# Kernel optimization log

Hardware: AMD Instinct MI355X
Metric: run time of the kernel (lower is better)

The kernel has to match this reference:

```python
import jax, jax.numpy as jnp
import numpy as np

N_NODES = 50000
N_EDGES = 800000
D_IN = 128
D_OUT = 128


def setup_inputs() -> dict:
    key = jax.random.key(0)
    k1, k2, k3, k4, k5, k6 = jax.random.split(key, 6)
    curr_fea = jax.random.normal(k1, (N_NODES, D_IN), dtype=jnp.float32)
    edge_index = jax.random.randint(k2, (2, N_EDGES), 0, N_NODES, dtype=jnp.int64)
    s = 1.0 / np.sqrt(D_IN)
    W_self = jax.random.uniform(k3, (D_OUT, D_IN), jnp.float32, -s, s)
    b_self = jax.random.uniform(k4, (D_OUT,), jnp.float32, -s, s)
    W_neig = jax.random.uniform(k5, (D_OUT, D_IN), jnp.float32, -s, s)
    b_neig = jax.random.uniform(k6, (D_OUT,), jnp.float32, -s, s)
    return {"curr_fea": curr_fea, "edge_index": edge_index,
            "W_self": W_self, "b_self": b_self,
            "W_neig": W_neig, "b_neig": b_neig}


def reference(curr_fea, edge_index, W_self, b_self, W_neig, b_neig):
    num_nodes = curr_fea.shape[0]
    src, dst = edge_index[0], edge_index[1]
    # symmetrize: messages flow both directions
    src_all = jnp.concatenate([src, dst], axis=0)  # [2E]
    dst_all = jnp.concatenate([dst, src], axis=0)  # [2E]
    # gather neighbor features then scatter-add into destination nodes
    nei_sum = jax.ops.segment_sum(curr_fea[src_all], dst_all,
                                  num_segments=num_nodes)  # [N, d]
    out = (curr_fea @ W_self.T + b_self) + (nei_sum @ W_neig.T + b_neig)
    return out
```

## Files before the change

kernel.cpp:

```cpp
#include <hip/hip_runtime.h>

#define DD 128
#define BM 64
#define BK 32
#define BKN 64
#define NPB 32
#define NBMAX 1024
#define ECH 2048
#define CAP 2304
#define PADC 136

typedef __attribute__((ext_vector_type(8))) short bf16x8;
typedef __attribute__((ext_vector_type(4))) float f32x4;

__device__ __forceinline__ unsigned short f2b(float x) {
    unsigned u = __float_as_uint(x);
    u += 0x7fffu + ((u >> 16) & 1u);
    return (unsigned short)(u >> 16);
}
__device__ __forceinline__ float b2f_lo(unsigned v) { return __uint_as_float(v << 16); }
__device__ __forceinline__ float b2f_hi(unsigned v) { return __uint_as_float(v & 0xffff0000u); }
__device__ __forceinline__ float bf(unsigned short u) {
    return __uint_as_float((unsigned)u << 16);
}

__device__ __forceinline__ int detect_rf(const void* ei_raw, int E, int lane) {
    const unsigned long long* p = (const unsigned long long*)ei_raw;
    int n64 = E < 64 ? E : 64;
    bool big = (lane < n64) && (p[lane] >= (1ULL << 32));
    return (__ballot(big) == 0ULL) ? 1 : 0;
}

__global__ void detect_kernel(const unsigned long long* __restrict__ ei,
                              int n64, int* __restrict__ flag) {
    int i = threadIdx.x;
    bool big = (i < n64) && (ei[i] >= (1ULL << 32));
    unsigned long long b = __ballot(big);
    if (i == 0) *flag = (b == 0ULL) ? 1 : 0;
}

__global__ void cvt_all_kernel(const float* __restrict__ fea,
                               const float* __restrict__ Ws,
                               const float* __restrict__ Wn,
                               unsigned short* __restrict__ feaB,
                               unsigned short* __restrict__ Wcat, int n4) {
    int i = blockIdx.x * 256 + threadIdx.x;
    if (i < n4) {
        float4 v = reinterpret_cast<const float4*>(fea)[i];
        ushort4 o;
        o.x = f2b(v.x); o.y = f2b(v.y); o.z = f2b(v.z); o.w = f2b(v.w);
        reinterpret_cast<ushort4*>(feaB)[i] = o;
    } else if (i < n4 + 2 * DD * DD / 4) {
        int k4 = i - n4;
        int n = k4 >> 6;
        int kk = (k4 & 63) * 4;
        float4 v = (kk < DD) ? *reinterpret_cast<const float4*>(Ws + n * DD + kk)
                             : *reinterpret_cast<const float4*>(Wn + n * DD + kk - DD);
        ushort4 o;
        o.x = f2b(v.x); o.y = f2b(v.y); o.z = f2b(v.z); o.w = f2b(v.w);
        reinterpret_cast<ushort4*>(Wcat)[k4] = o;
    }
}

__global__ void cvt_fea_kernel(const float* __restrict__ in,
                               unsigned short* __restrict__ out, int n4) {
    int i = blockIdx.x * 256 + threadIdx.x;
    if (i >= n4) return;
    float4 v = reinterpret_cast<const float4*>(in)[i];
    ushort4 o;
    o.x = f2b(v.x); o.y = f2b(v.y); o.z = f2b(v.z); o.w = f2b(v.w);
    reinterpret_cast<ushort4*>(out)[i] = o;
}

__global__ void cvt_w_kernel(const float* __restrict__ Ws,
                             const float* __restrict__ Wn,
                             unsigned short* __restrict__ Wcat) {
    int i = blockIdx.x * 256 + threadIdx.x;
    int n = i >> 8, k = i & 255;
    float v = (k < DD) ? Ws[n * DD + k] : Wn[n * DD + (k - DD)];
    Wcat[i] = f2b(v);
}

__launch_bounds__(512)
__global__ void bin_kernel(const void* __restrict__ ei_raw, int E,
                           unsigned* __restrict__ region,
                           unsigned* __restrict__ gcur, int nbk) {
    __shared__ unsigned stage[2 * ECH];
    __shared__ unsigned cnt[NBMAX];
    __shared__ unsigned start[NBMAX];
    __shared__ unsigned cursor[NBMAX];
    __shared__ unsigned gbase[NBMAX];
    __shared__ unsigned scanT[512];

    const int t = threadIdx.x;
    const int lane = t & 63;
    const int rf = detect_rf(ei_raw, E, lane);

    for (int b = t; b < NBMAX; b += 512) { cnt[b] = 0; cursor[b] = 0; }
    __syncthreads();

    const int e0 = blockIdx.x * ECH;
    int es[4], ed[4];
#pragma unroll
    for (int j = 0; j < 4; ++j) {
        int e = e0 + j * 512 + t;
        if (e < E) {
            if (rf) {
                const long long* p = (const long long*)ei_raw;
                es[j] = (int)p[e]; ed[j] = (int)p[e + E];
            } else {
                const int* p = (const int*)ei_raw;
                es[j] = p[e]; ed[j] = p[e + E];
            }
            atomicAdd(&cnt[ed[j] >> 6], 1u);
            atomicAdd(&cnt[es[j] >> 6], 1u);
        } else {
            es[j] = -1; ed[j] = -1;
        }
    }
    __syncthreads();

    unsigned lv[2]; unsigned lsum = 0;
#pragma unroll
    for (int j = 0; j < 2; ++j) { lv[j] = cnt[t * 2 + j]; lsum += lv[j]; }
    scanT[t] = lsum; __syncthreads();
    for (int o = 1; o < 512; o <<= 1) {
        unsigned x = (t >= o) ? scanT[t - o] : 0;
        __syncthreads();
        scanT[t] += x;
        __syncthreads();
    }
    unsigned run = scanT[t] - lsum;
#pragma unroll
    for (int j = 0; j < 2; ++j) { start[t * 2 + j] = run; run += lv[j]; }
    __syncthreads();

#pragma unroll
    for (int j = 0; j < 4; ++j) {
        if (es[j] >= 0) {
            int s = es[j], d = ed[j];
            unsigned p0 = atomicAdd(&cursor[d >> 6], 1u);
            stage[start[d >> 6] + p0] = (unsigned)(d & 63) | ((unsigned)s << 6);
            unsigned p1 = atomicAdd(&cursor[s >> 6], 1u);
            stage[start[s >> 6] + p1] = (unsigned)(s & 63) | ((unsigned)d << 6);
        }
    }
    __syncthreads();

    for (int b = t; b < nbk; b += 512) {
        unsigned c = cnt[b];
        gbase[b] = c ? atomicAdd(&gcur[b], c) : 0;
    }
    __syncthreads();

    const int w = t >> 6;
    for (int b = w; b < nbk; b += 8) {
        unsigned c = cnt[b];
        if (!c) continue;
        unsigned gb = gbase[b], st = start[b];
        for (unsigned l2 = lane; l2 < c; l2 += 64) {
            unsigned idx = gb + l2;
            if (idx < CAP)
                region[(size_t)b * CAP + idx] = stage[st + l2];
        }
    }
}

__launch_bounds__(256)
__global__ void gather_gemm2_kernel(const unsigned short* __restrict__ feaB,
                                    const unsigned short* __restrict__ Wcat,
                                    const unsigned* __restrict__ region,
                                    const unsigned* __restrict__ gcur,
                                    const float* __restrict__ bs,
                                    const float* __restrict__ bn,
                                    float* __restrict__ out, int M) {
    __shared__ unsigned srt[CAP];
    __shared__ unsigned short neiL[NPB][PADC];
    __shared__ unsigned c64[BKN];
    __shared__ unsigned p64[BKN];
    __shared__ unsigned cur64[BKN];

    const int t = threadIdx.x;
    const int b2 = blockIdx.x, b = b2 >> 1, h = b2 & 1;
    unsigned cnt = gcur[b];
    if (cnt > CAP) cnt = CAP;
    const unsigned* reg = region + (size_t)b * CAP;

    unsigned ent[9];
#pragma unroll
    for (int q = 0; q < 9; ++q) {
        unsigned i = (unsigned)t + (unsigned)q * 256u;
        ent[q] = (i < cnt) ? reg[i] : 0xFFFFFFFFu;
    }

    if (t < BKN) { c64[t] = 0; cur64[t] = 0; }
    __syncthreads();

#pragma unroll
    for (int q = 0; q < 9; ++q)
        if (ent[q] != 0xFFFFFFFFu) atomicAdd(&c64[ent[q] & 63u], 1u);
    __syncthreads();

    if (t < 64) {
        unsigned v = c64[t];
        unsigned sc = v;
#pragma unroll
        for (int o = 1; o < 64; o <<= 1) {
            unsigned x = __shfl_up(sc, o, 64);
            if (t >= o) sc += x;
        }
        p64[t] = sc - v;
    }
    __syncthreads();

#pragma unroll
    for (int q = 0; q < 9; ++q) {
        if (ent[q] != 0xFFFFFFFFu) {
            unsigned e = ent[q];
            unsigned p = atomicAdd(&cur64[e & 63u], 1u);
            srt[p64[e & 63u] + p] = e >> 6;
        }
    }
    __syncthreads();

    const int w = t >> 6, lane = t & 63;
    const int half = lane >> 5, li = lane & 31;
    const unsigned short* bp = feaB + li * 4;

    for (int n = h * NPB + w; n < h * NPB + NPB; n += 4) {
        int g = b * BKN + n;
        unsigned p = p64[n];
        unsigned d = (g < M) ? c64[n] : 0;
        float a0 = 0.f, a1 = 0.f, a2 = 0.f, a3 = 0.f;
        unsigned j = 0;
        for (; j + 16 <= d; j += 16) {
            ushort4 v[8];
#pragma unroll
            for (int q = 0; q < 8; ++q) {
                unsigned s = srt[p + j + 2 * q + half];
                v[q] = *reinterpret_cast<const ushort4*>(bp + (size_t)s * DD);
            }
#pragma unroll
            for (int q = 0; q < 8; ++q) {
                a0 += bf(v[q].x); a1 += bf(v[q].y);
                a2 += bf(v[q].z); a3 += bf(v[q].w);
            }
        }
        for (; j + 2 <= d; j += 2) {
            unsigned s = srt[p + j + half];
            ushort4 v = *reinterpret_cast<const ushort4*>(bp + (size_t)s * DD);
            a0 += bf(v.x); a1 += bf(v.y); a2 += bf(v.z); a3 += bf(v.w);
        }
        if (j < d && half == 0) {
            unsigned s = srt[p + j];
            ushort4 v = *reinterpret_cast<const ushort4*>(bp + (size_t)s * DD);
            a0 += bf(v.x); a1 += bf(v.y); a2 += bf(v.z); a3 += bf(v.w);
        }
        a0 += __shfl_xor(a0, 32);
        a1 += __shfl_xor(a1, 32);
        a2 += __shfl_xor(a2, 32);
        a3 += __shfl_xor(a3, 32);
        if (half == 0) {
            ushort4 o;
            o.x = f2b(a0); o.y = f2b(a1); o.z = f2b(a2); o.w = f2b(a3);
            *reinterpret_cast<ushort4*>(&neiL[n - h * NPB][li * 4]) = o;
        }
    }
    __syncthreads();

    const int lr = lane & 15, ks = lane >> 4;
    const int rg = w & 1, cgr = w >> 1;
    const int row0 = b2 * NPB + rg * 16;
    const int rowl = rg * 16 + lr;
    const int rowg = row0 + lr;
    const int col0 = cgr * 64;

    f32x4 acc[4] = {};
#pragma unroll
    for (int kb = 0; kb < 256; kb += 32) {
        bf16x8 a;
        if (kb < DD) {
            if (rowg < M)
                a = *reinterpret_cast<const bf16x8*>(
                    feaB + (size_t)rowg * DD + kb + ks * 8);
            else
                a = bf16x8{0, 0, 0, 0, 0, 0, 0, 0};
        } else {
            a = *reinterpret_cast<const bf16x8*>(&neiL[rowl][(kb - DD) + ks * 8]);
        }
#pragma unroll
        for (int ci = 0; ci < 4; ++ci) {
            int nn = col0 + ci * 16 + lr;
            bf16x8 bb = *reinterpret_cast<const bf16x8*>(
                Wcat + (size_t)nn * 256 + kb + ks * 8);
            acc[ci] = __builtin_amdgcn_mfma_f32_16x16x32_bf16(a, bb, acc[ci], 0, 0, 0);
        }
    }

#pragma unroll
    for (int ci = 0; ci < 4; ++ci) {
        int colg = col0 + ci * 16 + lr;
        float bias = bs[colg] + bn[colg];
        int rbase = row0 + ks * 4;
#pragma unroll
        for (int i2 = 0; i2 < 4; ++i2) {
            int r2 = rbase + i2;
            if (r2 < M) out[(size_t)r2 * DD + colg] = acc[ci][i2] + bias;
        }
    }
}

__global__ void transpose_kernel(const float* __restrict__ Ws,
                                 const float* __restrict__ Wn,
                                 float* __restrict__ Wts,
                                 float* __restrict__ Wtn) {
    int idx = blockIdx.x * blockDim.x + threadIdx.x;
    int i = idx & (DD * DD - 1);
    int col = i >> 7;
    int k = i & (DD - 1);
    if (idx < DD * DD)          Wts[k * DD + col] = Ws[i];
    else if (idx < 2 * DD * DD) Wtn[k * DD + col] = Wn[i];
}

__global__ void hist_kernel(const void* __restrict__ ei_raw,
                            int* __restrict__ deg, int E,
                            const int* __restrict__ flag) {
    int e = blockIdx.x * 256 + threadIdx.x;
    if (e >= E) return;
    int s, d;
    if (*flag) {
        const long long* ei = (const long long*)ei_raw;
        s = (int)ei[e]; d = (int)ei[e + E];
    } else {
        const int* ei = (const int*)ei_raw;
        s = ei[e]; d = ei[e + E];
    }
    atomicAdd(&deg[s], 1);
    atomicAdd(&deg[d], 1);
}

__global__ void scan1_kernel(const int* __restrict__ deg, int* __restrict__ off,
                             int* __restrict__ bsum, int N) {
    __shared__ int sd[256];
    int base = blockIdx.x * 1024;
    int t = threadIdx.x;
    int v[4]; int s = 0;
#pragma unroll
    for (int j = 0; j < 4; ++j) {
        int idx = base + t * 4 + j;
        v[j] = (idx < N) ? deg[idx] : 0;
        s += v[j];
    }
    sd[t] = s; __syncthreads();
    for (int o = 1; o < 256; o <<= 1) {
        int x = (t >= o) ? sd[t - o] : 0;
        __syncthreads();
        sd[t] += x;
        __syncthreads();
    }
    int run = sd[t] - s;
    if (t == 255) bsum[blockIdx.x] = sd[255];
#pragma unroll
    for (int j = 0; j < 4; ++j) {
        int idx = base + t * 4 + j;
        if (idx < N) off[idx] = run;
        run += v[j];
    }
}

__global__ void scan2_kernel(int* __restrict__ bsum, int NB,
                             int* __restrict__ total) {
    __shared__ int sd[256];
    int t = threadIdx.x;
    int v = (t < NB) ? bsum[t] : 0;
    sd[t] = v; __syncthreads();
    for (int o = 1; o < 256; o <<= 1) {
        int x = (t >= o) ? sd[t - o] : 0;
        __syncthreads();
        sd[t] += x;
        __syncthreads();
    }
    if (t < NB) bsum[t] = sd[t] - v;
    if (t == 255) *total = sd[255];
}

__global__ void scan3_kernel(int* __restrict__ off, const int* __restrict__ bsum,
                             int N) {
    int i = blockIdx.x * blockDim.x + threadIdx.x;
    if (i < N) off[i] += bsum[i >> 10];
}

__global__ void fill_kernel(const void* __restrict__ ei_raw,
                            const int* __restrict__ off,
                            int* __restrict__ cursor, int* __restrict__ list,
                            int E, const int* __restrict__ flag) {
    int e = blockIdx.x * 256 + threadIdx.x;
    if (e >= E) return;
    int s, d;
    if (*flag) {
        const long long* ei = (const long long*)ei_raw;
        s = (int)ei[e]; d = (int)ei[e + E];
    } else {
        const int* ei = (const int*)ei_raw;
        s = ei[e]; d = ei[e + E];
    }
    int p0 = atomicAdd(&cursor[d], 1); list[off[d] + p0] = s;
    int p1 = atomicAdd(&cursor[s], 1); list[off[s] + p1] = d;
}

__launch_bounds__(256)
__global__ void gather_b_kernel(const unsigned short* __restrict__ feaB,
                                const int* __restrict__ off,
                                const int* __restrict__ list,
                                unsigned short* __restrict__ neiB, int N) {
    int w = (int)((blockIdx.x * 256 + threadIdx.x) >> 6);
    if (w >= N) return;
    int lane = threadIdx.x & 63;
    int start = off[w], end = off[w + 1];
    float ax = 0.f, ay = 0.f;
    const unsigned short* base = feaB + lane * 2;
    int j = start;
    for (; j + 4 <= end; j += 4) {
        int s0 = list[j], s1 = list[j + 1], s2 = list[j + 2], s3 = list[j + 3];
        unsigned a = *reinterpret_cast<const unsigned*>(base + (size_t)s0 * DD);
        unsigned b = *reinterpret_cast<const unsigned*>(base + (size_t)s1 * DD);
        unsigned c = *reinterpret_cast<const unsigned*>(base + (size_t)s2 * DD);
        unsigned d = *reinterpret_cast<const unsigned*>(base + (size_t)s3 * DD);
        ax += b2f_lo(a) + b2f_lo(b) + b2f_lo(c) + b2f_lo(d);
        ay += b2f_hi(a) + b2f_hi(b) + b2f_hi(c) + b2f_hi(d);
    }
    for (; j < end; ++j) {
        unsigned a = *reinterpret_cast<const unsigned*>(base + (size_t)list[j] * DD);
        ax += b2f_lo(a); ay += b2f_hi(a);
    }
    ushort2 o; o.x = f2b(ax); o.y = f2b(ay);
    *reinterpret_cast<ushort2*>(neiB + (size_t)w * DD + lane * 2) = o;
}

__launch_bounds__(256)
__global__ void gather_f32_kernel(const float* __restrict__ fea,
                                  const int* __restrict__ off,
                                  const int* __restrict__ list,
                                  float* __restrict__ nei, int N) {
    int w = (int)((blockIdx.x * 256 + threadIdx.x) >> 6);
    if (w >= N) return;
    int lane = threadIdx.x & 63;
    int start = off[w], end = off[w + 1];
    float2 acc = make_float2(0.f, 0.f);
    const float* base = fea + (size_t)lane * 2;
    int j = start;
    for (; j + 4 <= end; j += 4) {
        int s0 = list[j], s1 = list[j + 1], s2 = list[j + 2], s3 = list[j + 3];
        float2 a = *reinterpret_cast<const float2*>(base + (size_t)s0 * DD);
        float2 b = *reinterpret_cast<const float2*>(base + (size_t)s1 * DD);
        float2 c = *reinterpret_cast<const float2*>(base + (size_t)s2 * DD);
        float2 e = *reinterpret_cast<const float2*>(base + (size_t)s3 * DD);
        acc.x += a.x + b.x + c.x + e.x;
        acc.y += a.y + b.y + c.y + e.y;
    }
    for (; j < end; ++j) {
        float2 a = *reinterpret_cast<const float2*>(base + (size_t)list[j] * DD);
        acc.x += a.x; acc.y += a.y;
    }
    *reinterpret_cast<float2*>(nei + (size_t)w * DD + lane * 2) = acc;
}

__global__ void scatter_kernel(const float* __restrict__ fea,
                               const void* __restrict__ ei_raw,
                               float* __restrict__ nei,
                               int E, const int* __restrict__ flag) {
    long long r = (long long)blockIdx.x * 8 + (threadIdx.x >> 5);
    if (r >= 2LL * E) return;
    int lr = threadIdx.x & 31;
    int i = (int)(r < E ? r : r - E);
    int s, d;
    if (*flag) {
        const long long* ei = (const long long*)ei_raw;
        s = (int)ei[i]; d = (int)ei[i + E];
    } else {
        const int* ei = (const int*)ei_raw;
        s = ei[i]; d = ei[i + E];
    }
    if (r >= E) { int t = s; s = d; d = t; }
    const float4 v = *reinterpret_cast<const float4*>(fea + (size_t)s * DD + lr * 4);
    float* p = nei + (size_t)d * DD + lr * 4;
    unsafeAtomicAdd(p + 0, v.x);
    unsafeAtomicAdd(p + 1, v.y);
    unsafeAtomicAdd(p + 2, v.z);
    unsafeAtomicAdd(p + 3, v.w);
}

__launch_bounds__(256)
__global__ void gemm_mfma_kernel(const unsigned short* __restrict__ feaB,
                                 const unsigned short* __restrict__ neiB,
                                 const unsigned short* __restrict__ Wcat,
                                 const float* __restrict__ bs,
                                 const float* __restrict__ bn,
                                 float* __restrict__ out, int M) {
    const int w  = threadIdx.x >> 6;
    const int l  = threadIdx.x & 63;
    const int lr = l & 15;
    const int ks = l >> 4;
    const int row0 = blockIdx.x * 128 + w * 32;
    const int col0 = blockIdx.y * 64;

    f32x4 acc[2][4] = {};

#pragma unroll
    for (int kb = 0; kb < 256; kb += 32) {
        const unsigned short* A = (kb < DD) ? feaB : neiB;
        const int klocal = (kb < DD) ? kb : kb - DD;
        bf16x8 a[2];
#pragma unroll
        for (int ri = 0; ri < 2; ++ri) {
            int rowg = row0 + ri * 16 + lr;
            if (rowg < M)
                a[ri] = *reinterpret_cast<const bf16x8*>(
                    A + (size_t)rowg * DD + klocal + ks * 8);
            else
                a[ri] = bf16x8{0, 0, 0, 0, 0, 0, 0, 0};
        }
#pragma unroll
        for (int ci = 0; ci < 4; ++ci) {
            int n = col0 + ci * 16 + lr;
            bf16x8 b = *reinterpret_cast<const bf16x8*>(
                Wcat + (size_t)n * 256 + kb + ks * 8);
#pragma unroll
            for (int ri = 0; ri < 2; ++ri)
                acc[ri][ci] = __builtin_amdgcn_mfma_f32_16x16x32_bf16(
                    a[ri], b, acc[ri][ci], 0, 0, 0);
        }
    }

#pragma unroll
    for (int ci = 0; ci < 4; ++ci) {
        int colg = col0 + ci * 16 + lr;
        float bias = bs[colg] + bn[colg];
#pragma unroll
        for (int ri = 0; ri < 2; ++ri) {
            int rbase = row0 + ri * 16 + ks * 4;
#pragma unroll
            for (int i = 0; i < 4; ++i) {
                int rowg = rbase + i;
                if (rowg < M)
                    out[(size_t)rowg * DD + colg] = acc[ri][ci][i] + bias;
            }
        }
    }
}

__launch_bounds__(256)
__global__ void gemm_kernel(const float* __restrict__ fea,
                            const float* __restrict__ nei,
                            const float* __restrict__ Wts,
                            const float* __restrict__ Wtn,
                            const float* __restrict__ bs,
                            const float* __restrict__ bn,
                            float* __restrict__ out, int M) {
    __shared__ float Fs[BM][BK + 4];
    __shared__ float Ns[BM][BK + 4];
    __shared__ float WsT[BK][DD];
    __shared__ float WnT[BK][DD];

    const int t = threadIdx.x;
    const int cg = t & 31;
    const int rg = t >> 5;
    const int row0 = blockIdx.x * BM;

    float4 acc[8];
#pragma unroll
    for (int r = 0; r < 8; ++r) acc[r] = make_float4(0.f, 0.f, 0.f, 0.f);

    for (int kb = 0; kb < DD; kb += BK) {
#pragma unroll
        for (int j = 0; j < 2; ++j) {
            int idx = t + j * 256;
            int row = idx >> 3;
            int seg = idx & 7;
            int grow = row0 + row;
            float4 fv = make_float4(0.f, 0.f, 0.f, 0.f);
            float4 nv = make_float4(0.f, 0.f, 0.f, 0.f);
            if (grow < M) {
                fv = *reinterpret_cast<const float4*>(fea + (size_t)grow * DD + kb + seg * 4);
                nv = *reinterpret_cast<const float4*>(nei + (size_t)grow * DD + kb + seg * 4);
            }
            *reinterpret_cast<float4*>(&Fs[row][seg * 4]) = fv;
            *reinterpret_cast<float4*>(&Ns[row][seg * 4]) = nv;
        }
#pragma unroll
        for (int j = 0; j < 4; ++j) {
            int idx = t + j * 256;
            int kk = idx >> 5;
            int seg = idx & 31;
            *reinterpret_cast<float4*>(&WsT[kk][seg * 4]) =
                *reinterpret_cast<const float4*>(Wts + (size_t)(kb + kk) * DD + seg * 4);
            *reinterpret_cast<float4*>(&WnT[kk][seg * 4]) =
                *reinterpret_cast<const float4*>(Wtn + (size_t)(kb + kk) * DD + seg * 4);
        }
        __syncthreads();

#pragma unroll
        for (int kk = 0; kk < BK; ++kk) {
            float4 wsv = *reinterpret_cast<const float4*>(&WsT[kk][cg * 4]);
            float4 wnv = *reinterpret_cast<const float4*>(&WnT[kk][cg * 4]);
#pragma unroll
            for (int r = 0; r < 8; ++r) {
                float a = Fs[rg * 8 + r][kk];
                float b = Ns[rg * 8 + r][kk];
                acc[r].x += a * wsv.x + b * wnv.x;
                acc[r].y += a * wsv.y + b * wnv.y;
                acc[r].z += a * wsv.z + b * wnv.z;
                acc[r].w += a * wsv.w + b * wnv.w;
            }
        }
        __syncthreads();
    }

    float4 bsv = *reinterpret_cast<const float4*>(bs + cg * 4);
    float4 bnv = *reinterpret_cast<const float4*>(bn + cg * 4);
    float4 bias = make_float4(bsv.x + bnv.x, bsv.y + bnv.y, bsv.z + bnv.z, bsv.w + bnv.w);
#pragma unroll
    for (int r = 0; r < 8; ++r) {
        int grow = row0 + rg * 8 + r;
        if (grow < M) {
            float4 o = make_float4(acc[r].x + bias.x, acc[r].y + bias.y,
                                   acc[r].z + bias.z, acc[r].w + bias.w);
            *reinterpret_cast<float4*>(out + (size_t)grow * DD + cg * 4) = o;
        }
    }
}

extern "C" void kernel_launch(void* const* d_in, const int* in_sizes, int n_in,
                              void* d_out, int out_size, void* d_ws, size_t ws_size,
                              hipStream_t stream) {
    const float* fea = (const float*)d_in[0];
    const void*  ei  = d_in[1];
    const float* Ws  = (const float*)d_in[2];
    const float* bsv = (const float*)d_in[3];
    const float* Wn  = (const float*)d_in[4];
    const float* bnv = (const float*)d_in[5];

    const int M = in_sizes[0] / DD;
    const int E = in_sizes[1] / 2;
    float* out = (float*)d_out;
    char* ws = (char*)d_ws;
    int* flag = (int*)ws;

    const int NBK = (M + BKN - 1) / BKN;
    const size_t csr_bytes = (size_t)M * 8 + (size_t)(M + 1) * 4 + 4096
                           + (size_t)2 * E * 4;

    size_t o1 = 256;
    unsigned short* Wcat = (unsigned short*)(ws + o1); o1 += (size_t)DD * 256 * 2;
    unsigned short* feaB = (unsigned short*)(ws + o1); o1 += (size_t)M * DD * 2;
    unsigned* gcur  = (unsigned*)(ws + o1);            o1 += 4096;
    unsigned* region = (unsigned*)(ws + o1);           o1 += (size_t)NBK * CAP * 4;
    size_t need1 = o1;

    size_t o2 = 256 + (size_t)DD * 256 * 2 + (size_t)M * DD * 2;
    unsigned short* neiB2 = (unsigned short*)(ws + o2);
    size_t o2b = o2 + (size_t)M * DD * 2;
    size_t need2 = o2b + csr_bytes;

    size_t o3 = 256;
    float* Wts = (float*)(ws + o3); o3 += (size_t)DD * DD * 4;
    float* Wtn = (float*)(ws + o3); o3 += (size_t)DD * DD * 4;
    size_t need3 = o3 + csr_bytes;

    const int NB = (M + 1023) / 1024;
    const int eb = (E + 255) / 256;
    const int n4 = M * DD / 4;

    if (ws_size >= need1 && NBK <= NBMAX) {
        hipMemsetAsync(gcur, 0, 4096, stream);
        int cvtb = (n4 + 2 * DD * DD / 4 + 255) / 256;
        cvt_all_kernel<<<cvtb, 256, 0, stream>>>(fea, Ws, Wn, feaB, Wcat, n4);
        int abks = (E + ECH - 1) / ECH;
        bin_kernel<<<abks, 512, 0, stream>>>(ei, E, region, gcur, NBK);
        gather_gemm2_kernel<<<2 * NBK, 256, 0, stream>>>(feaB, Wcat, region, gcur,
                                                         bsv, bnv, out, M);
    } else if (ws_size >= need2) {
        int* deg    = (int*)(ws + o2b);
        int* cursor = deg + M;
        int* off    = cursor + M;
        int* bsum   = off + (M + 1);
        int* list   = bsum + 1024;

        detect_kernel<<<1, 64, 0, stream>>>((const unsigned long long*)ei,
                                            E < 64 ? E : 64, flag);
        cvt_fea_kernel<<<(n4 + 255) / 256, 256, 0, stream>>>(fea, feaB, n4);
        cvt_w_kernel<<<(DD * 256 + 255) / 256, 256, 0, stream>>>(Ws, Wn, Wcat);
        hipMemsetAsync(deg, 0, (size_t)2 * M * 4, stream);
        hist_kernel<<<eb, 256, 0, stream>>>(ei, deg, E, flag);
        scan1_kernel<<<NB, 256, 0, stream>>>(deg, off, bsum, M);
        scan2_kernel<<<1, 256, 0, stream>>>(bsum, NB, &off[M]);
        scan3_kernel<<<(M + 255) / 256, 256, 0, stream>>>(off, bsum, M);
        fill_kernel<<<eb, 256, 0, stream>>>(ei, off, cursor, list, E, flag);
        gather_b_kernel<<<(M + 3) / 4, 256, 0, stream>>>(feaB, off, list, neiB2, M);
        dim3 g((M + 127) / 128, 2);
        gemm_mfma_kernel<<<g, 256, 0, stream>>>(feaB, neiB2, Wcat, bsv, bnv, out, M);
    } else if (ws_size >= need3) {
        int* deg    = (int*)(ws + o3);
        int* cursor = deg + M;
        int* off    = cursor + M;
        int* bsum   = off + (M + 1);
        int* list   = bsum + 1024;
        float* nei = out;

        detect_kernel<<<1, 64, 0, stream>>>((const unsigned long long*)ei,
                                            E < 64 ? E : 64, flag);
        transpose_kernel<<<(2 * DD * DD + 255) / 256, 256, 0, stream>>>(Ws, Wn, Wts, Wtn);
        hipMemsetAsync(deg, 0, (size_t)2 * M * 4, stream);
        hist_kernel<<<eb, 256, 0, stream>>>(ei, deg, E, flag);
        scan1_kernel<<<NB, 256, 0, stream>>>(deg, off, bsum, M);
        scan2_kernel<<<1, 256, 0, stream>>>(bsum, NB, &off[M]);
        scan3_kernel<<<(M + 255) / 256, 256, 0, stream>>>(off, bsum, M);
        fill_kernel<<<eb, 256, 0, stream>>>(ei, off, cursor, list, E, flag);
        gather_f32_kernel<<<(M + 3) / 4, 256, 0, stream>>>(fea, off, list, nei, M);
        gemm_kernel<<<(M + BM - 1) / BM, 256, 0, stream>>>(fea, nei, Wts, Wtn,
                                                           bsv, bnv, out, M);
    } else {
        float* nei = out;
        detect_kernel<<<1, 64, 0, stream>>>((const unsigned long long*)ei,
                                            E < 64 ? E : 64, flag);
        transpose_kernel<<<(2 * DD * DD + 255) / 256, 256, 0, stream>>>(Ws, Wn, Wts, Wtn);
        hipMemsetAsync(nei, 0, (size_t)M * DD * 4, stream);
        long long rows = 2LL * E;
        int sblocks = (int)((rows + 7) / 8);
        scatter_kernel<<<sblocks, 256, 0, stream>>>(fea, ei, nei, E, flag);
        gemm_kernel<<<(M + BM - 1) / BM, 256, 0, stream>>>(fea, nei, Wts, Wtn,
                                                           bsv, bnv, out, M);
    }
}
```

Measured before the change: 199.6 us.

## Fuse bf16 conversion into binning kernel and widen neighbor gather loads

```diff
diff --git a/kernel.cpp b/kernel.cpp
--- a/kernel.cpp
+++ b/kernel.cpp
@@ -12,6 +12,7 @@
 
 typedef __attribute__((ext_vector_type(8))) short bf16x8;
 typedef __attribute__((ext_vector_type(4))) float f32x4;
+typedef __attribute__((ext_vector_type(8))) unsigned short u16x8;
 
 __device__ __forceinline__ unsigned short f2b(float x) {
     unsigned u = __float_as_uint(x);
@@ -37,29 +38,6 @@
     bool big = (i < n64) && (ei[i] >= (1ULL << 32));
     unsigned long long b = __ballot(big);
     if (i == 0) *flag = (b == 0ULL) ? 1 : 0;
-}
-
-__global__ void cvt_all_kernel(const float* __restrict__ fea,
-                               const float* __restrict__ Ws,
-                               const float* __restrict__ Wn,
-                               unsigned short* __restrict__ feaB,
-                               unsigned short* __restrict__ Wcat, int n4) {
-    int i = blockIdx.x * 256 + threadIdx.x;
-    if (i < n4) {
-        float4 v = reinterpret_cast<const float4*>(fea)[i];
-        ushort4 o;
-        o.x = f2b(v.x); o.y = f2b(v.y); o.z = f2b(v.z); o.w = f2b(v.w);
-        reinterpret_cast<ushort4*>(feaB)[i] = o;
-    } else if (i < n4 + 2 * DD * DD / 4) {
-        int k4 = i - n4;
-        int n = k4 >> 6;
-        int kk = (k4 & 63) * 4;
-        float4 v = (kk < DD) ? *reinterpret_cast<const float4*>(Ws + n * DD + kk)
-                             : *reinterpret_cast<const float4*>(Wn + n * DD + kk - DD);
-        ushort4 o;
-        o.x = f2b(v.x); o.y = f2b(v.y); o.z = f2b(v.z); o.w = f2b(v.w);
-        reinterpret_cast<ushort4*>(Wcat)[k4] = o;
-    }
 }
 
 __global__ void cvt_fea_kernel(const float* __restrict__ in,
@@ -82,9 +60,14 @@
 }
 
 __launch_bounds__(512)
-__global__ void bin_kernel(const void* __restrict__ ei_raw, int E,
-                           unsigned* __restrict__ region,
-                           unsigned* __restrict__ gcur, int nbk) {
+__global__ void binc_kernel(const void* __restrict__ ei_raw, int E,
+                            unsigned* __restrict__ region,
+                            unsigned* __restrict__ gcur, int nbk, int abks,
+                            const float* __restrict__ fea,
+                            const float* __restrict__ Ws,
+                            const float* __restrict__ Wn,
+                            unsigned short* __restrict__ feaB,
+                            unsigned short* __restrict__ Wcat, int n4) {
     __shared__ unsigned stage[2 * ECH];
     __shared__ unsigned cnt[NBMAX];
     __shared__ unsigned start[NBMAX];
@@ -93,6 +76,27 @@
     __shared__ unsigned scanT[512];
 
     const int t = threadIdx.x;
+
+    if (blockIdx.x >= abks) {
+        int i = (blockIdx.x - abks) * 512 + t;
+        if (i < n4) {
+            float4 v = reinterpret_cast<const float4*>(fea)[i];
+            ushort4 o;
+            o.x = f2b(v.x); o.y = f2b(v.y); o.z = f2b(v.z); o.w = f2b(v.w);
+            reinterpret_cast<ushort4*>(feaB)[i] = o;
+        } else if (i < n4 + 2 * DD * DD / 4) {
+            int k4 = i - n4;
+            int n = k4 >> 6;
+            int kk = (k4 & 63) * 4;
+            float4 v = (kk < DD) ? *reinterpret_cast<const float4*>(Ws + n * DD + kk)
+                                 : *reinterpret_cast<const float4*>(Wn + n * DD + kk - DD);
+            ushort4 o;
+            o.x = f2b(v.x); o.y = f2b(v.y); o.z = f2b(v.z); o.w = f2b(v.w);
+            reinterpret_cast<ushort4*>(Wcat)[k4] = o;
+        }
+        return;
+    }
+
     const int lane = t & 63;
     const int rf = detect_rf(ei_raw, E, lane);
 
@@ -224,49 +228,65 @@
     __syncthreads();
 
     const int w = t >> 6, lane = t & 63;
-    const int half = lane >> 5, li = lane & 31;
-    const unsigned short* bp = feaB + li * 4;
+    const int grp = lane >> 4, li16 = lane & 15;
+    const unsigned short* bp = feaB + li16 * 8;
 
     for (int n = h * NPB + w; n < h * NPB + NPB; n += 4) {
         int g = b * BKN + n;
         unsigned p = p64[n];
         unsigned d = (g < M) ? c64[n] : 0;
-        float a0 = 0.f, a1 = 0.f, a2 = 0.f, a3 = 0.f;
+        float a[8] = {0.f, 0.f, 0.f, 0.f, 0.f, 0.f, 0.f, 0.f};
         unsigned j = 0;
+        for (; j + 32 <= d; j += 32) {
+            u16x8 v[8];
+#pragma unroll
+            for (int q = 0; q < 8; ++q) {
+                unsigned s = srt[p + j + 4 * q + grp];
+                v[q] = *reinterpret_cast<const u16x8*>(bp + (size_t)s * DD);
+            }
+#pragma unroll
+            for (int q = 0; q < 8; ++q) {
+#pragma unroll
+                for (int c = 0; c < 8; ++c) a[c] += bf(v[q][c]);
+            }
+        }
         for (; j + 16 <= d; j += 16) {
-            ushort4 v[8];
-#pragma unroll
-            for (int q = 0; q < 8; ++q) {
-                unsigned s = srt[p + j + 2 * q + half];
-                v[q] = *reinterpret_cast<const ushort4*>(bp + (size_t)s * DD);
+            u16x8 v[4];
+#pragma unroll
+            for (int q = 0; q < 4; ++q) {
+                unsigned s = srt[p + j + 4 * q + grp];
+                v[q] = *reinterpret_cast<const u16x8*>(bp + (size_t)s * DD);
             }
 #pragma unroll
-            for (int q = 0; q < 8; ++q) {
-                a0 += bf(v[q].x); a1 += bf(v[q].y);
-                a2 += bf(v[q].z); a3 += bf(v[q].w);
+            for (int q = 0; q < 4; ++q) {
+#pragma unroll
+                for (int c = 0; c < 8; ++c) a[c] += bf(v[q][c]);
             }
         }
-        for (; j + 2 <= d; j += 2) {
-            unsigned s = srt[p + j + half];
-            ushort4 v = *reinterpret_cast<const ushort4*>(bp + (size_t)s * DD);
-            a0 += bf(v.x); a1 += bf(v.y); a2 += bf(v.z); a3 += bf(v.w);
-        }
-        if (j < d && half == 0) {
-            unsigned s = srt[p + j];
-            ushort4 v = *reinterpret_cast<const ushort4*>(bp + (size_t)s * DD);
-            a0 += bf(v.x); a1 += bf(v.y); a2 += bf(v.z); a3 += bf(v.w);
-        }
-        a0 += __shfl_xor(a0, 32);
-        a1 += __shfl_xor(a1, 32);
-        a2 += __shfl_xor(a2, 32);
-        a3 += __shfl_xor(a3, 32);
-        if (half == 0) {
-            ushort4 o;
-            o.x = f2b(a0); o.y = f2b(a1); o.z = f2b(a2); o.w = f2b(a3);
-            *reinterpret_cast<ushort4*>(&neiL[n - h * NPB][li * 4]) = o;
-        }
-    }
-    __syncthreads();
+        for (; j + 4 <= d; j += 4) {
+            unsigned s = srt[p + j + grp];
+            u16x8 v = *reinterpret_cast<const u16x8*>(bp + (size_t)s * DD);
+#pragma unroll
+            for (int c = 0; c < 8; ++c) a[c] += bf(v[c]);
+        }
+        if (j < d && grp < (int)(d - j)) {
+            unsigned s = srt[p + j + grp];
+            u16x8 v = *reinterpret_cast<const u16x8*>(bp + (size_t)s * DD);
+#pragma unroll
+            for (int c = 0; c < 8; ++c) a[c] += bf(v[c]);
+        }
+#pragma unroll
+        for (int c = 0; c < 8; ++c) {
+            a[c] += __shfl_xor(a[c], 16);
+            a[c] += __shfl_xor(a[c], 32);
+        }
+        if (grp == 0) {
+            u16x8 o;
+#pragma unroll
+            for (int c = 0; c < 8; ++c) o[c] = f2b(a[c]);
+            *reinterpret_cast<u16x8*>(&neiL[n - h * NPB][li16 * 8]) = o;
+        }
+    }
 
     const int lr = lane & 15, ks = lane >> 4;
     const int rg = w & 1, cgr = w >> 1;
@@ -277,23 +297,31 @@
 
     f32x4 acc[4] = {};
 #pragma unroll
-    for (int kb = 0; kb < 256; kb += 32) {
-        bf16x8 a;
-        if (kb < DD) {
-            if (rowg < M)
-                a = *reinterpret_cast<const bf16x8*>(
-                    feaB + (size_t)rowg * DD + kb + ks * 8);
-            else
-                a = bf16x8{0, 0, 0, 0, 0, 0, 0, 0};
-        } else {
-            a = *reinterpret_cast<const bf16x8*>(&neiL[rowl][(kb - DD) + ks * 8]);
-        }
+    for (int kb = 0; kb < DD; kb += 32) {
+        bf16x8 av;
+        if (rowg < M)
+            av = *reinterpret_cast<const bf16x8*>(
+                feaB + (size_t)rowg * DD + kb + ks * 8);
+        else
+            av = bf16x8{0, 0, 0, 0, 0, 0, 0, 0};
 #pragma unroll
         for (int ci = 0; ci < 4; ++ci) {
             int nn = col0 + ci * 16 + lr;
             bf16x8 bb = *reinterpret_cast<const bf16x8*>(
                 Wcat + (size_t)nn * 256 + kb + ks * 8);
-            acc[ci] = __builtin_amdgcn_mfma_f32_16x16x32_bf16(a, bb, acc[ci], 0, 0, 0);
+            acc[ci] = __builtin_amdgcn_mfma_f32_16x16x32_bf16(av, bb, acc[ci], 0, 0, 0);
+        }
+    }
+    __syncthreads();
+#pragma unroll
+    for (int kb = DD; kb < 256; kb += 32) {
+        bf16x8 av = *reinterpret_cast<const bf16x8*>(&neiL[rowl][(kb - DD) + ks * 8]);
+#pragma unroll
+        for (int ci = 0; ci < 4; ++ci) {
+            int nn = col0 + ci * 16 + lr;
+            bf16x8 bb = *reinterpret_cast<const bf16x8*>(
+                Wcat + (size_t)nn * 256 + kb + ks * 8);
+            acc[ci] = __builtin_amdgcn_mfma_f32_16x16x32_bf16(av, bb, acc[ci], 0, 0, 0);
         }
     }
 
@@ -673,10 +701,11 @@
 
     if (ws_size >= need1 && NBK <= NBMAX) {
         hipMemsetAsync(gcur, 0, 4096, stream);
-        int cvtb = (n4 + 2 * DD * DD / 4 + 255) / 256;
-        cvt_all_kernel<<<cvtb, 256, 0, stream>>>(fea, Ws, Wn, feaB, Wcat, n4);
         int abks = (E + ECH - 1) / ECH;
-        bin_kernel<<<abks, 512, 0, stream>>>(ei, E, region, gcur, NBK);
+        int cvtb = (n4 + 2 * DD * DD / 4 + 511) / 512;
+        binc_kernel<<<abks + cvtb, 512, 0, stream>>>(ei, E, region, gcur, NBK,
+                                                     abks, fea, Ws, Wn, feaB,
+                                                     Wcat, n4);
         gather_gemm2_kernel<<<2 * NBK, 256, 0, stream>>>(feaB, Wcat, region, gcur,
                                                          bsv, bnv, out, M);
     } else if (ws_size >= need2) {
```

Measured after the change: 200.8 us. About the same (+0.6%).
